# Optimization experiments

Hardware: AMD Instinct MI355X
Metric: run time of the kernel (lower is better)

Reference implementation:

```python
import jax, jax.numpy as jnp
import numpy as np

VOCAB, D_MODEL, N_STATE, H_HEADS, LAYERS = 64, 512, 32, 16, 4
EXPAND = 2
D_INNER = EXPAND * D_MODEL          # 1024
P_HEAD = D_INNER // H_HEADS         # 64
CONV_DIM = D_INNER + 2 * N_STATE    # x, B, C share the depthwise conv
K_CONV = 4
D_IN_PROJ = 2 * D_INNER + 2 * N_STATE + H_HEADS  # z, x, B, C, dt
BATCH, SEQ = 4, 1024
EPS = 1e-5


def rmsnorm(x, w):
    return x * jax.lax.rsqrt(jnp.mean(x * x, axis=-1, keepdims=True) + EPS) * w


def silu(x):
    return x * jax.nn.sigmoid(x)


def causal_depthwise_conv(x, w, b):
    # x: [B,L,C], w: [C,K], b: [C]; causal (left) padding, depthwise groups
    xt = jnp.transpose(x, (0, 2, 1))  # [B,C,L]
    out = jax.lax.conv_general_dilated(xt, w[:, None, :], (1,), [(K_CONV - 1, 0)], feature_group_count=w.shape[0])
    return jnp.transpose(out, (0, 2, 1)) + b


def ssd(xh, dt, A, Bm, Cm, Dp):
    # Mamba2 SSD recurrence. xh [B,L,H,P], dt [B,L,H], A [H], Bm/Cm [B,L,N], Dp [H]
    dA = jnp.exp(dt * A)              # decay per (batch, step, head)
    dtx = dt[..., None] * xh          # [B,L,H,P]

    def step(h, inp):
        dA_t, dtx_t, B_t, C_t = inp
        # h: [B,H,P,N]
        h = dA_t[:, :, None, None] * h + dtx_t[..., None] * B_t[:, None, None, :]
        y = jnp.einsum('bhpn,bn->bhp', h, C_t)
        return h, y

    h0 = jnp.zeros((xh.shape[0], H_HEADS, P_HEAD, N_STATE), xh.dtype)
    _, ys = jax.lax.scan(step, h0, (jnp.moveaxis(dA, 1, 0), jnp.moveaxis(dtx, 1, 0), jnp.moveaxis(Bm, 1, 0), jnp.moveaxis(Cm, 1, 0)))
    return jnp.moveaxis(ys, 0, 1) + xh * Dp[None, None, :, None]


def mamba_block(x, norm_w, W_in, b_in, conv_w, conv_b, dt_bias, A_log, Dp, gnorm_w, W_out, b_out):
    res = x
    u = rmsnorm(x, norm_w)
    zxbcdt = u @ W_in + b_in                                # [B,L,D_IN_PROJ]
    z = zxbcdt[..., :D_INNER]
    xBC = zxbcdt[..., D_INNER:D_INNER + CONV_DIM]
    dt = zxbcdt[..., D_INNER + CONV_DIM:]                   # [B,L,H]
    xBC = silu(causal_depthwise_conv(xBC, conv_w, conv_b))
    xc = xBC[..., :D_INNER]
    Bm = xBC[..., D_INNER:D_INNER + N_STATE]
    Cm = xBC[..., D_INNER + N_STATE:]
    dt = jax.nn.softplus(dt + dt_bias)
    xh = xc.reshape(xc.shape[0], xc.shape[1], H_HEADS, P_HEAD)
    y = ssd(xh, dt, -jnp.exp(A_log), Bm, Cm, Dp)
    y = y.reshape(y.shape[0], y.shape[1], D_INNER)
    y = rmsnorm(y * silu(z), gnorm_w)                       # gated RMSNorm
    return res + y @ W_out + b_out


def forward(input_tokens, emb, norm_w, W_in, b_in, conv_w, conv_b, dt_bias, A_log, D_param, gnorm_w, W_out, b_out, head_w, head_b):
    h = emb[input_tokens]
    for i in range(LAYERS):
        h = mamba_block(h, norm_w[i], W_in[i], b_in[i], conv_w[i], conv_b[i], dt_bias[i], A_log[i], D_param[i], gnorm_w[i], W_out[i], b_out[i])
    return h @ head_w + head_b


def setup_inputs() -> dict:
    key = jax.random.key(0)
    ks = jax.random.split(key, 8)
    s = 0.02
    return {
        'input_tokens': jax.random.randint(ks[0], (BATCH, SEQ), 0, VOCAB),
        'emb': jax.random.normal(ks[1], (VOCAB, D_MODEL), jnp.float32) * s,
        'norm_w': jnp.ones((LAYERS, D_MODEL), jnp.float32),
        'W_in': jax.random.normal(ks[2], (LAYERS, D_MODEL, D_IN_PROJ), jnp.float32) * s,
        'b_in': jnp.zeros((LAYERS, D_IN_PROJ), jnp.float32),
        'conv_w': jax.random.normal(ks[3], (LAYERS, CONV_DIM, K_CONV), jnp.float32) * 0.1,
        'conv_b': jnp.zeros((LAYERS, CONV_DIM), jnp.float32),
        'dt_bias': jnp.tile(jnp.log(jnp.expm1(jnp.linspace(0.001, 0.1, H_HEADS, dtype=jnp.float32))), (LAYERS, 1)),
        'A_log': jnp.tile(jnp.log(jnp.arange(1, H_HEADS + 1, dtype=jnp.float32)), (LAYERS, 1)),
        'D_param': jnp.ones((LAYERS, H_HEADS), jnp.float32),
        'gnorm_w': jnp.ones((LAYERS, D_INNER), jnp.float32),
        'W_out': jax.random.normal(ks[4], (LAYERS, D_INNER, D_MODEL), jnp.float32) * s,
        'b_out': jnp.zeros((LAYERS, D_MODEL), jnp.float32),
        'head_w': jax.random.normal(ks[5], (D_MODEL, VOCAB), jnp.float32) * s,
        'head_b': jnp.zeros((VOCAB,), jnp.float32),
    }


def reference(input_tokens, emb, norm_w, W_in, b_in, conv_w, conv_b, dt_bias, A_log, D_param, gnorm_w, W_out, b_out, head_w, head_b):
    return forward(input_tokens, emb, norm_w, W_in, b_in, conv_w, conv_b, dt_bias, A_log, D_param, gnorm_w, W_out, b_out, head_w, head_b)
```

## Files before the change

kernel.cpp:

```cpp
#include <hip/hip_runtime.h>
#include <hip/hip_bf16.h>

#define VOCAB     64
#define D_MODEL   512
#define N_STATE   32
#define H_HEADS   16
#define LAYERS    4
#define D_INNER   1024
#define P_HEAD    64
#define CONV_DIM  1088
#define K_CONV    4
#define D_IN_PROJ 2128
#define NPAD_IN   2176
#define NPAD_HEAD 64
#define BATCH     4
#define SEQ       1024
#define NTOK      (BATCH*SEQ)
#define EPS       1e-5f
#define CL        64
#define NC        (SEQ/CL)
#define PSTR      80

typedef __bf16 bf16x8 __attribute__((ext_vector_type(8)));
typedef float  f32x4  __attribute__((ext_vector_type(4)));

__device__ __forceinline__ float sigmoidf_(float x) { return 1.f / (1.f + __expf(-x)); }
__device__ __forceinline__ float softplusf_(float x) { return (x > 20.f) ? x : log1pf(__expf(x)); }

__device__ __forceinline__ void gload_lds16(const void* g, void* l) {
  __builtin_amdgcn_global_load_lds((const __attribute__((address_space(1))) void*)g,
                                   (__attribute__((address_space(3))) void*)l,
                                   16, 0, 0);
}

__global__ __launch_bounds__(256) void rmsnorm512_kernel(
    const float* __restrict__ x, const float* __restrict__ w,
    __bf16* __restrict__ out,
    const int* __restrict__ tok, const float* __restrict__ emb,
    float* __restrict__ hout) {
  int wv = threadIdx.x >> 6, lane = threadIdx.x & 63;
  int tokid = blockIdx.x * 4 + wv;
  const float* src = tok ? emb + (size_t)tok[tokid] * D_MODEL
                         : x + (size_t)tokid * D_MODEL;
  f32x4 v0 = *(const f32x4*)(src + lane * 8);
  f32x4 v1 = *(const f32x4*)(src + lane * 8 + 4);
  if (tok) {
    float* hr = hout + (size_t)tokid * D_MODEL;
    *(f32x4*)(hr + lane * 8) = v0;
    *(f32x4*)(hr + lane * 8 + 4) = v1;
  }
  float ss = v0[0]*v0[0] + v0[1]*v0[1] + v0[2]*v0[2] + v0[3]*v0[3]
           + v1[0]*v1[0] + v1[1]*v1[1] + v1[2]*v1[2] + v1[3]*v1[3];
  #pragma unroll
  for (int o = 32; o >= 1; o >>= 1) ss += __shfl_xor(ss, o);
  float sc = rsqrtf(ss * (1.f / D_MODEL) + EPS);
  f32x4 w0 = *(const f32x4*)(w + lane * 8);
  f32x4 w1 = *(const f32x4*)(w + lane * 8 + 4);
  bf16x8 o8;
  #pragma unroll
  for (int k = 0; k < 4; k++) o8[k]     = (__bf16)(v0[k] * sc * w0[k]);
  #pragma unroll
  for (int k = 0; k < 4; k++) o8[4 + k] = (__bf16)(v1[k] * sc * w1[k]);
  *(bf16x8*)(out + (size_t)tokid * D_MODEL + lane * 8) = o8;
}

__global__ __launch_bounds__(256) void transpose_all_kernel(
    const float* __restrict__ W_in, const float* __restrict__ W_out,
    const float* __restrict__ head_w,
    __bf16* __restrict__ WtIn, __bf16* __restrict__ WtOut, __bf16* __restrict__ WtHead) {
  int b = blockIdx.x;
  const float* W; __bf16* Wt; int K, N, Npad, bx, by;
  if (b < 4352) {
    int z = b / 1088, r = b % 1088;
    bx = r % 68; by = r / 68;
    W = W_in + (size_t)z * D_MODEL * D_IN_PROJ;
    Wt = WtIn + (size_t)z * NPAD_IN * D_MODEL;
    K = D_MODEL; N = D_IN_PROJ; Npad = NPAD_IN;
  } else if (b < 6400) {
    int r = b - 4352; int z = r / 512; r %= 512;
    bx = r % 16; by = r / 16;
    W = W_out + (size_t)z * D_INNER * D_MODEL;
    Wt = WtOut + (size_t)z * D_MODEL * D_INNER;
    K = D_INNER; N = D_MODEL; Npad = D_MODEL;
  } else {
    int r = b - 6400;
    bx = r % 2; by = r / 2;
    W = head_w; Wt = WtHead;
    K = D_MODEL; N = VOCAB; Npad = NPAD_HEAD;
  }
  __shared__ float T[32][33];
  int n0 = bx * 32, k0 = by * 32;
  int tx = threadIdx.x & 31, ty = threadIdx.x >> 5;
  #pragma unroll
  for (int i = 0; i < 4; i++) {
    int n = n0 + tx;
    T[ty + i * 8][tx] = (n < N) ? W[(size_t)(k0 + ty + i * 8) * N + n] : 0.f;
  }
  __syncthreads();
  #pragma unroll
  for (int i = 0; i < 4; i++)
    Wt[(size_t)(n0 + ty + i * 8) * K + k0 + tx] = (__bf16)T[tx][ty + i * 8];
}

#define TK 64
__global__ __launch_bounds__(256) void gemm_bf16_kernel(
    const __bf16* __restrict__ A, const __bf16* __restrict__ Bt,
    const float* __restrict__ bias, const float* __restrict__ res,
    float* __restrict__ C, __bf16* __restrict__ Cbf, int K, int N, int ldc) {
  __shared__ __bf16 As[64 * TK];
  __shared__ __bf16 Bs[64 * TK];
  int tid = threadIdx.x;
  int lane = tid & 63, wave = tid >> 6;
  int wm = wave >> 1, wn = wave & 1;
  int q = lane >> 4, l16 = lane & 15;
  size_t row0 = (size_t)blockIdx.y * 64;
  int col0 = blockIdx.x * 64;
  const __bf16* Ab = A + row0 * K;
  const __bf16* Bb = Bt + (size_t)col0 * K;

  f32x4 acc[2][2];
  #pragma unroll
  for (int i = 0; i < 2; i++)
    #pragma unroll
    for (int j = 0; j < 2; j++) acc[i][j] = (f32x4){0.f, 0.f, 0.f, 0.f};

  for (int k0 = 0; k0 < K; k0 += TK) {
    #pragma unroll
    for (int r = 0; r < 2; r++) {
      int lin = r * 256 + tid;
      size_t goff = (size_t)(lin >> 3) * K + k0 + (lin & 7) * 8;
      gload_lds16(Ab + goff, As + lin * 8);
      gload_lds16(Bb + goff, Bs + lin * 8);
    }
    __syncthreads();
    #pragma unroll
    for (int ks = 0; ks < 2; ks++) {
      bf16x8 af[2], bfv[2];
      #pragma unroll
      for (int i = 0; i < 2; i++)
        af[i] = *(const bf16x8*)(As + (wm * 32 + i * 16 + l16) * TK + ks * 32 + q * 8);
      #pragma unroll
      for (int j = 0; j < 2; j++)
        bfv[j] = *(const bf16x8*)(Bs + (wn * 32 + j * 16 + l16) * TK + ks * 32 + q * 8);
      #pragma unroll
      for (int i = 0; i < 2; i++)
        #pragma unroll
        for (int j = 0; j < 2; j++)
          acc[i][j] = __builtin_amdgcn_mfma_f32_16x16x32_bf16(af[i], bfv[j], acc[i][j], 0, 0, 0);
    }
    __syncthreads();
  }

  #pragma unroll
  for (int i = 0; i < 2; i++) {
    size_t mrow = row0 + wm * 32 + i * 16 + q * 4;
    #pragma unroll
    for (int j = 0; j < 2; j++) {
      int col = col0 + wn * 32 + j * 16 + l16;
      if (col < N) {
        float bv = bias ? bias[col] : 0.f;
        #pragma unroll
        for (int rr = 0; rr < 4; rr++) {
          size_t off = (mrow + rr) * (size_t)ldc + col;
          float v = acc[i][j][rr] + bv;
          if (res) v += res[off];
          if (C)   C[off] = v;
          if (Cbf) Cbf[off] = (__bf16)v;
        }
      }
    }
  }
}

__global__ __launch_bounds__(256) void gemm_bf16_128(
    const __bf16* __restrict__ A, const __bf16* __restrict__ Bt,
    const float* __restrict__ bias, __bf16* __restrict__ Cbf,
    int K, int N, int ldc) {
  __shared__ __bf16 As[128 * TK];
  __shared__ __bf16 Bs[128 * TK];
  int tid = threadIdx.x;
  int lane = tid & 63, wave = tid >> 6;
  int wm = wave >> 1, wn = wave & 1;
  int q = lane >> 4, l16 = lane & 15;
  size_t row0 = (size_t)blockIdx.y * 128;
  int col0 = blockIdx.x * 128;
  const __bf16* Ab = A + row0 * K;
  const __bf16* Bb = Bt + (size_t)col0 * K;

  f32x4 acc[4][4];
  #pragma unroll
  for (int i = 0; i < 4; i++)
    #pragma unroll
    for (int j = 0; j < 4; j++) acc[i][j] = (f32x4){0.f, 0.f, 0.f, 0.f};

  for (int k0 = 0; k0 < K; k0 += TK) {
    #pragma unroll
    for (int r = 0; r < 4; r++) {
      int lin = r * 256 + tid;
      size_t goff = (size_t)(lin >> 3) * K + k0 + (lin & 7) * 8;
      gload_lds16(Ab + goff, As + lin * 8);
      gload_lds16(Bb + goff, Bs + lin * 8);
    }
    __syncthreads();
    #pragma unroll
    for (int ks = 0; ks < 2; ks++) {
      bf16x8 af[4], bfv[4];
      #pragma unroll
      for (int i = 0; i < 4; i++)
        af[i] = *(const bf16x8*)(As + (wm * 64 + i * 16 + l16) * TK + ks * 32 + q * 8);
      #pragma unroll
      for (int j = 0; j < 4; j++)
        bfv[j] = *(const bf16x8*)(Bs + (wn * 64 + j * 16 + l16) * TK + ks * 32 + q * 8);
      #pragma unroll
      for (int i = 0; i < 4; i++)
        #pragma unroll
        for (int j = 0; j < 4; j++)
          acc[i][j] = __builtin_amdgcn_mfma_f32_16x16x32_bf16(af[i], bfv[j], acc[i][j], 0, 0, 0);
    }
    __syncthreads();
  }

  #pragma unroll
  for (int i = 0; i < 4; i++) {
    size_t mrow = row0 + wm * 64 + i * 16 + q * 4;
    #pragma unroll
    for (int j = 0; j < 4; j++) {
      int col = col0 + wn * 64 + j * 16 + l16;
      if (col < N) {
        float bv = bias[col];
        #pragma unroll
        for (int rr = 0; rr < 4; rr++)
          Cbf[(mrow + rr) * (size_t)ldc + col] = (__bf16)(acc[i][j][rr] + bv);
      }
    }
  }
}

__device__ __forceinline__ void wave0_dt_cumsum(
    const __bf16* __restrict__ zxbf, const float* __restrict__ dt_bias,
    int b, int h, int t0, int tid, float* ldt, float* lcs) {
  if (tid < 64) {
    float dv = (float)zxbf[((size_t)(b * SEQ + t0 + tid)) * D_IN_PROJ + 2 * D_INNER + 2 * N_STATE + h]
               + dt_bias[h];
    float dtv = softplusf_(dv);
    float cs = dtv;
    #pragma unroll
    for (int off = 1; off < 64; off <<= 1) {
      float o = __shfl_up(cs, off);
      if (tid >= off) cs += o;
    }
    ldt[tid] = dtv;
    lcs[tid] = cs;
  }
}

__global__ __launch_bounds__(256) void ssd_local_kernel(
    const __bf16* __restrict__ zxbf, const float* __restrict__ conv_w,
    const float* __restrict__ conv_b, const float* __restrict__ dt_bias,
    const float* __restrict__ A_log,
    float* __restrict__ Slocal, float* __restrict__ dAprod) {
  int blk = blockIdx.x;
  int c = blk % NC;
  int h = (blk / NC) % H_HEADS;
  int b = blk / (NC * H_HEADS);
  int tid = threadIdx.x;
  int lane = tid & 63, wave = tid >> 6;
  int q = lane >> 4, l16 = lane & 15;
  int t0 = c * CL;
  float A = -__expf(A_log[h]);
  __shared__ __bf16 rawbuf[68 * 64 + 68 * 32];
  __shared__ __bf16 lxT[64][PSTR];
  __shared__ __bf16 lBT[32][PSTR];
  __shared__ float ldt[64], lcs[64];
  __bf16* rawx = rawbuf;
  __bf16* rawB = rawbuf + 68 * 64;
  for (int i = tid; i < 68 * 8; i += 256) {
    int r = i >> 3, c0 = (i & 7) * 8;
    int gr = t0 - 3 + r;
    bf16x8 v;
    #pragma unroll
    for (int k = 0; k < 8; k++) v[k] = (__bf16)0.f;
    if (gr >= 0)
      v = *(const bf16x8*)(zxbf + ((size_t)(b * SEQ + gr)) * D_IN_PROJ + D_INNER + h * 64 + c0);
    *(bf16x8*)(rawx + r * 64 + c0) = v;
  }
  for (int i = tid; i < 68 * 4; i += 256) {
    int r = i >> 2, c0 = (i & 3) * 8;
    int gr = t0 - 3 + r;
    bf16x8 v;
    #pragma unroll
    for (int k = 0; k < 8; k++) v[k] = (__bf16)0.f;
    if (gr >= 0)
      v = *(const bf16x8*)(zxbf + ((size_t)(b * SEQ + gr)) * D_IN_PROJ + 2 * D_INNER + c0);
    *(bf16x8*)(rawB + r * 32 + c0) = v;
  }
  wave0_dt_cumsum(zxbf, dt_bias, b, h, t0, tid, ldt, lcs);
  __syncthreads();
  float cs63 = lcs[63];
  {
    int p = tid & 63;
    const float* w = conv_w + (h * 64 + p) * K_CONV;
    float w0 = w[0], w1 = w[1], w2 = w[2], w3 = w[3];
    float cb = conv_b[h * 64 + p];
    for (int i = tid; i < CL * 64; i += 256) {
      int t = i >> 6;
      float a = cb + w0 * (float)rawx[t * 64 + p] + w1 * (float)rawx[(t + 1) * 64 + p]
                   + w2 * (float)rawx[(t + 2) * 64 + p] + w3 * (float)rawx[(t + 3) * 64 + p];
      lxT[p][t] = (__bf16)(a * sigmoidf_(a));
    }
  }
  {
    int n = tid & 31;
    const float* w = conv_w + (D_INNER + n) * K_CONV;
    float w0 = w[0], w1 = w[1], w2 = w[2], w3 = w[3];
    float cb = conv_b[D_INNER + n];
    for (int i = tid; i < CL * 32; i += 256) {
      int t = i >> 5;
      float a = cb + w0 * (float)rawB[t * 32 + n] + w1 * (float)rawB[(t + 1) * 32 + n]
                   + w2 * (float)rawB[(t + 2) * 32 + n] + w3 * (float)rawB[(t + 3) * 32 + n];
      float v = a * sigmoidf_(a);
      float wt = ldt[t] * __expf(A * (cs63 - lcs[t]));
      lBT[n][t] = (__bf16)(v * wt);
    }
  }
  __syncthreads();
  f32x4 acc[2];
  acc[0] = (f32x4){0.f,0.f,0.f,0.f}; acc[1] = (f32x4){0.f,0.f,0.f,0.f};
  #pragma unroll
  for (int kb = 0; kb < 2; kb++) {
    bf16x8 af = *(const bf16x8*)(&lxT[wave * 16 + l16][kb * 32 + q * 8]);
    #pragma unroll
    for (int j = 0; j < 2; j++) {
      bf16x8 bf = *(const bf16x8*)(&lBT[l16 + 16 * j][kb * 32 + q * 8]);
      acc[j] = __builtin_amdgcn_mfma_f32_16x16x32_bf16(af, bf, acc[j], 0, 0, 0);
    }
  }
  float* sT = (float*)rawbuf;
  #pragma unroll
  for (int j = 0; j < 2; j++) {
    int n = l16 + 16 * j;
    #pragma unroll
    for (int rr = 0; rr < 4; rr++) {
      int p = wave * 16 + q * 4 + rr;
      sT[p * 36 + n] = acc[j][rr];
    }
  }
  {
    int row = tid >> 2, c0 = (tid & 3) * 8;
    f32x4 a = *(const f32x4*)(sT + row * 36 + c0);
    f32x4 b2 = *(const f32x4*)(sT + row * 36 + c0 + 4);
    float* dstp = Slocal + (size_t)blk * 2048 + row * 32 + c0;
    *(f32x4*)dstp = a;
    *(f32x4*)(dstp + 4) = b2;
  }
  if (tid == 0) dAprod[blk] = __expf(A * cs63);
}

__global__ __launch_bounds__(256) void ssd_out_kernel(
    const __bf16* __restrict__ zxbf, const float* __restrict__ conv_w,
    const float* __restrict__ conv_b, const float* __restrict__ dt_bias,
    const float* __restrict__ A_log, const float* __restrict__ Dp,
    const float* __restrict__ Slocal, const float* __restrict__ dAprod,
    __bf16* __restrict__ y) {
  int blk = blockIdx.x;
  int c = blk % NC;
  int h = (blk / NC) % H_HEADS;
  int b = blk / (NC * H_HEADS);
  int tid = threadIdx.x;
  int lane = tid & 63, wave = tid >> 6;
  int q = lane >> 4, l16 = lane & 15;
  int t0 = c * CL;
  float A = -__expf(A_log[h]);
  float D = Dp[h];
  __shared__ __bf16 rawbuf[2 * 68 * 64];
  __shared__ __bf16 lxT[64][PSTR];
  __shared__ __bf16 lB[64][32];
  __shared__ __bf16 lC[64][32];
  __shared__ __bf16 lS[64][32];
  __shared__ float ldt[64], lcs[64];
  __shared__ float pr[NC];
  __bf16* rawx = rawbuf;
  __bf16* rawBC = rawbuf + 68 * 64;
  for (int i = tid; i < 68 * 8; i += 256) {
    int r = i >> 3, c0 = (i & 7) * 8;
    int gr = t0 - 3 + r;
    bf16x8 vx, vbc;
    #pragma unroll
    for (int k = 0; k < 8; k++) { vx[k] = (__bf16)0.f; vbc[k] = (__bf16)0.f; }
    if (gr >= 0) {
      const __bf16* rowp = zxbf + ((size_t)(b * SEQ + gr)) * D_IN_PROJ;
      vx  = *(const bf16x8*)(rowp + D_INNER + h * 64 + c0);
      vbc = *(const bf16x8*)(rowp + 2 * D_INNER + c0);
    }
    *(bf16x8*)(rawx + r * 64 + c0)  = vx;
    *(bf16x8*)(rawBC + r * 64 + c0) = vbc;
  }
  if (tid < NC) pr[tid] = dAprod[(blk - c) + tid];
  wave0_dt_cumsum(zxbf, dt_bias, b, h, t0, tid, ldt, lcs);
  __syncthreads();
  {
    int p = tid & 63;
    const float* w = conv_w + (h * 64 + p) * K_CONV;
    float w0 = w[0], w1 = w[1], w2 = w[2], w3 = w[3];
    float cb = conv_b[h * 64 + p];
    for (int i = tid; i < CL * 64; i += 256) {
      int t = i >> 6;
      float a = cb + w0 * (float)rawx[t * 64 + p] + w1 * (float)rawx[(t + 1) * 64 + p]
                   + w2 * (float)rawx[(t + 2) * 64 + p] + w3 * (float)rawx[(t + 3) * 64 + p];
      lxT[p][t] = (__bf16)(a * sigmoidf_(a));
    }
  }
  {
    int col = tid & 63;
    const float* w = conv_w + (D_INNER + col) * K_CONV;
    float w0 = w[0], w1 = w[1], w2 = w[2], w3 = w[3];
    float cb = conv_b[D_INNER + col];
    for (int i = tid; i < CL * 64; i += 256) {
      int t = i >> 6;
      float a = cb + w0 * (float)rawBC[t * 64 + col] + w1 * (float)rawBC[(t + 1) * 64 + col]
                   + w2 * (float)rawBC[(t + 2) * 64 + col] + w3 * (float)rawBC[(t + 3) * 64 + col];
      float v = a * sigmoidf_(a);
      if (col < 32) lB[t][col] = (__bf16)v; else lC[t][col - 32] = (__bf16)v;
    }
  }
  {
    int p = tid >> 2, n0 = (tid & 3) * 8;
    const float* sl = Slocal + (size_t)(blk - c) * 2048 + p * 32 + n0;
    float st[8] = {};
    for (int j = 0; j < c; j++) {
      f32x4 a = *(const f32x4*)(sl + (size_t)j * 2048);
      f32x4 bq = *(const f32x4*)(sl + (size_t)j * 2048 + 4);
      float prj = pr[j];
      #pragma unroll
      for (int k = 0; k < 4; k++) { st[k] = prj * st[k] + a[k]; st[4 + k] = prj * st[4 + k] + bq[k]; }
    }
    #pragma unroll
    for (int k = 0; k < 8; k++) lS[p][n0 + k] = (__bf16)st[k];
  }
  __syncthreads();
  bf16x8 afC = *(const bf16x8*)(&lC[wave * 16 + l16][q * 8]);
  f32x4 accG[4], accI[4], accY[4];
  #pragma unroll
  for (int j = 0; j < 4; j++) {
    accG[j] = (f32x4){0.f,0.f,0.f,0.f};
    accI[j] = (f32x4){0.f,0.f,0.f,0.f};
    accY[j] = (f32x4){0.f,0.f,0.f,0.f};
  }
  #pragma unroll
  for (int j = 0; j < 4; j++) {
    bf16x8 bf = *(const bf16x8*)(&lB[l16 + 16 * j][q * 8]);
    accG[j] = __builtin_amdgcn_mfma_f32_16x16x32_bf16(afC, bf, accG[j], 0, 0, 0);
  }
  #pragma unroll
  for (int j = 0; j < 4; j++) {
    bf16x8 bf = *(const bf16x8*)(&lS[l16 + 16 * j][q * 8]);
    accI[j] = __builtin_amdgcn_mfma_f32_16x16x32_bf16(afC, bf, accI[j], 0, 0, 0);
  }
  __bf16* pP = rawbuf + wave * 16 * PSTR;
  #pragma unroll
  for (int j = 0; j < 4; j++) {
    int s = l16 + 16 * j;
    float css = lcs[s], dts = ldt[s];
    #pragma unroll
    for (int rr = 0; rr < 4; rr++) {
      int tl = q * 4 + rr;
      int t = wave * 16 + tl;
      float val = accG[j][rr] * __expf(A * (lcs[t] - css)) * dts;
      if (s == t) val += D;
      if (s > t) val = 0.f;
      pP[tl * PSTR + s] = (__bf16)val;
    }
  }
  #pragma unroll
  for (int kb = 0; kb < 2; kb++) {
    bf16x8 afP = *(const bf16x8*)(pP + l16 * PSTR + kb * 32 + q * 8);
    #pragma unroll
    for (int j = 0; j < 4; j++) {
      bf16x8 bf = *(const bf16x8*)(&lxT[l16 + 16 * j][kb * 32 + q * 8]);
      accY[j] = __builtin_amdgcn_mfma_f32_16x16x32_bf16(afP, bf, accY[j], 0, 0, 0);
    }
  }
  __syncthreads();
  __bf16* yT = rawbuf;
  #pragma unroll
  for (int rr = 0; rr < 4; rr++) {
    int t = wave * 16 + q * 4 + rr;
    float cumt = __expf(A * lcs[t]);
    #pragma unroll
    for (int j = 0; j < 4; j++) {
      int p = l16 + 16 * j;
      yT[t * 72 + p] = (__bf16)(accY[j][rr] + cumt * accI[j][rr]);
    }
  }
  {
    int row = tid >> 2, col0 = (tid & 3) * 16;
    bf16x8 o0 = *(const bf16x8*)(yT + row * 72 + col0);
    bf16x8 o1 = *(const bf16x8*)(yT + row * 72 + col0 + 8);
    __bf16* yrow = y + ((size_t)(b * SEQ + t0 + row)) * D_INNER + h * 64 + col0;
    *(bf16x8*)yrow = o0;
    *(bf16x8*)(yrow + 8) = o1;
  }
}

__global__ __launch_bounds__(256) void gate_norm_kernel(
    const __bf16* __restrict__ zxbf, const float* __restrict__ gw,
    const __bf16* __restrict__ y, __bf16* __restrict__ ybf) {
  int wv = threadIdx.x >> 6, lane = threadIdx.x & 63;
  int tokid = blockIdx.x * 4 + wv;
  const __bf16* zr = zxbf + (size_t)tokid * D_IN_PROJ + lane * 16;
  const __bf16* yr = y + (size_t)tokid * D_INNER + lane * 16;
  bf16x8 z0 = *(const bf16x8*)zr;
  bf16x8 z1 = *(const bf16x8*)(zr + 8);
  bf16x8 y0 = *(const bf16x8*)yr;
  bf16x8 y1 = *(const bf16x8*)(yr + 8);
  float g[16];
  float ss = 0.f;
  #pragma unroll
  for (int k = 0; k < 8; k++) {
    float zz = (float)z0[k];
    float gg = (float)y0[k] * zz * sigmoidf_(zz);
    g[k] = gg; ss += gg * gg;
  }
  #pragma unroll
  for (int k = 0; k < 8; k++) {
    float zz = (float)z1[k];
    float gg = (float)y1[k] * zz * sigmoidf_(zz);
    g[8 + k] = gg; ss += gg * gg;
  }
  #pragma unroll
  for (int o = 32; o >= 1; o >>= 1) ss += __shfl_xor(ss, o);
  float sc = rsqrtf(ss * (1.f / D_INNER) + EPS);
  f32x4 w0 = *(const f32x4*)(gw + lane * 16);
  f32x4 w1 = *(const f32x4*)(gw + lane * 16 + 4);
  f32x4 w2 = *(const f32x4*)(gw + lane * 16 + 8);
  f32x4 w3 = *(const f32x4*)(gw + lane * 16 + 12);
  bf16x8 o0, o1;
  #pragma unroll
  for (int k = 0; k < 4; k++) o0[k]     = (__bf16)(g[k]      * sc * w0[k]);
  #pragma unroll
  for (int k = 0; k < 4; k++) o0[4 + k] = (__bf16)(g[4 + k]  * sc * w1[k]);
  #pragma unroll
  for (int k = 0; k < 4; k++) o1[k]     = (__bf16)(g[8 + k]  * sc * w2[k]);
  #pragma unroll
  for (int k = 0; k < 4; k++) o1[4 + k] = (__bf16)(g[12 + k] * sc * w3[k]);
  __bf16* orow = ybf + (size_t)tokid * D_INNER + lane * 16;
  *(bf16x8*)orow = o0;
  *(bf16x8*)(orow + 8) = o1;
}

extern "C" void kernel_launch(void* const* d_in, const int* in_sizes, int n_in,
                              void* d_out, int out_size, void* d_ws, size_t ws_size,
                              hipStream_t stream) {
  const int*   tok     = (const int*)  d_in[0];
  const float* emb     = (const float*)d_in[1];
  const float* norm_w  = (const float*)d_in[2];
  const float* W_in    = (const float*)d_in[3];
  const float* b_in    = (const float*)d_in[4];
  const float* conv_w  = (const float*)d_in[5];
  const float* conv_b  = (const float*)d_in[6];
  const float* dt_bias = (const float*)d_in[7];
  const float* A_log   = (const float*)d_in[8];
  const float* D_par   = (const float*)d_in[9];
  const float* gnorm_w = (const float*)d_in[10];
  const float* W_out   = (const float*)d_in[11];
  const float* b_out   = (const float*)d_in[12];
  const float* head_w  = (const float*)d_in[13];
  const float* head_b  = (const float*)d_in[14];
  float* out = (float*)d_out;

  char* p = (char*)d_ws;
  auto alloc = [&](size_t bytes) { void* r = (void*)p; p += (bytes + 255) & ~(size_t)255; return r; };
  float*  h      = (float*) alloc((size_t)NTOK * D_MODEL * 4);
  float*  slocal = (float*) alloc((size_t)BATCH * H_HEADS * NC * P_HEAD * N_STATE * 4);
  float*  daprod = (float*) alloc((size_t)BATCH * H_HEADS * NC * 4);
  __bf16* y      = (__bf16*)alloc((size_t)NTOK * D_INNER * 2);
  __bf16* zxbf   = (__bf16*)alloc((size_t)NTOK * D_IN_PROJ * 2);
  __bf16* ubf    = (__bf16*)alloc((size_t)NTOK * D_MODEL * 2);
  __bf16* ybf    = (__bf16*)alloc((size_t)NTOK * D_INNER * 2);
  __bf16* hbf    = (__bf16*)alloc((size_t)NTOK * D_MODEL * 2);
  __bf16* WtIn   = (__bf16*)alloc((size_t)LAYERS * NPAD_IN * D_MODEL * 2);
  __bf16* WtOut  = (__bf16*)alloc((size_t)LAYERS * D_MODEL * D_INNER * 2);
  __bf16* WtHead = (__bf16*)alloc((size_t)NPAD_HEAD * D_MODEL * 2);

  transpose_all_kernel<<<6432, 256, 0, stream>>>(W_in, W_out, head_w, WtIn, WtOut, WtHead);

  for (int l = 0; l < LAYERS; l++) {
    rmsnorm512_kernel<<<NTOK / 4, 256, 0, stream>>>(
        h, norm_w + (size_t)l * D_MODEL, ubf,
        (l == 0) ? tok : nullptr, (l == 0) ? emb : nullptr, h);

    gemm_bf16_128<<<dim3(NPAD_IN / 128, NTOK / 128), 256, 0, stream>>>(
        ubf, WtIn + (size_t)l * NPAD_IN * D_MODEL, b_in + (size_t)l * D_IN_PROJ,
        zxbf, D_MODEL, D_IN_PROJ, D_IN_PROJ);

    ssd_local_kernel<<<BATCH * H_HEADS * NC, 256, 0, stream>>>(
        zxbf, conv_w + (size_t)l * CONV_DIM * K_CONV, conv_b + (size_t)l * CONV_DIM,
        dt_bias + (size_t)l * H_HEADS, A_log + (size_t)l * H_HEADS, slocal, daprod);
    ssd_out_kernel<<<BATCH * H_HEADS * NC, 256, 0, stream>>>(
        zxbf, conv_w + (size_t)l * CONV_DIM * K_CONV, conv_b + (size_t)l * CONV_DIM,
        dt_bias + (size_t)l * H_HEADS, A_log + (size_t)l * H_HEADS,
        D_par + (size_t)l * H_HEADS, slocal, daprod, y);

    gate_norm_kernel<<<NTOK / 4, 256, 0, stream>>>(zxbf, gnorm_w + (size_t)l * D_INNER, y, ybf);

    gemm_bf16_kernel<<<dim3(D_MODEL / 64, NTOK / 64), 256, 0, stream>>>(
        ybf, WtOut + (size_t)l * D_MODEL * D_INNER, b_out + (size_t)l * D_MODEL, h, h,
        (l == LAYERS - 1) ? hbf : nullptr, D_INNER, D_MODEL, D_MODEL);
  }

  gemm_bf16_kernel<<<dim3(NPAD_HEAD / 64, NTOK / 64), 256, 0, stream>>>(
      hbf, WtHead, head_b, nullptr, out, nullptr, D_MODEL, VOCAB, VOCAB);
}
```

Measured before the change: 489.4 us.

## Fold RMSNorm weights into GEMM weights and apply row scales in epilogues

```diff
diff --git a/kernel.cpp b/kernel.cpp
--- a/kernel.cpp
+++ b/kernel.cpp
@@ -33,59 +33,53 @@
                                    16, 0, 0);
 }
 
-__global__ __launch_bounds__(256) void rmsnorm512_kernel(
-    const float* __restrict__ x, const float* __restrict__ w,
-    __bf16* __restrict__ out,
+__global__ __launch_bounds__(256) void embed_kernel(
     const int* __restrict__ tok, const float* __restrict__ emb,
-    float* __restrict__ hout) {
+    float* __restrict__ h, __bf16* __restrict__ hbf, float* __restrict__ hssq) {
   int wv = threadIdx.x >> 6, lane = threadIdx.x & 63;
   int tokid = blockIdx.x * 4 + wv;
-  const float* src = tok ? emb + (size_t)tok[tokid] * D_MODEL
-                         : x + (size_t)tokid * D_MODEL;
-  f32x4 v0 = *(const f32x4*)(src + lane * 8);
-  f32x4 v1 = *(const f32x4*)(src + lane * 8 + 4);
-  if (tok) {
-    float* hr = hout + (size_t)tokid * D_MODEL;
-    *(f32x4*)(hr + lane * 8) = v0;
-    *(f32x4*)(hr + lane * 8 + 4) = v1;
-  }
+  const float* er = emb + (size_t)tok[tokid] * D_MODEL;
+  f32x4 v0 = *(const f32x4*)(er + lane * 8);
+  f32x4 v1 = *(const f32x4*)(er + lane * 8 + 4);
+  float* hr = h + (size_t)tokid * D_MODEL;
+  *(f32x4*)(hr + lane * 8) = v0;
+  *(f32x4*)(hr + lane * 8 + 4) = v1;
+  bf16x8 o8;
+  #pragma unroll
+  for (int k = 0; k < 4; k++) { o8[k] = (__bf16)v0[k]; o8[4 + k] = (__bf16)v1[k]; }
+  *(bf16x8*)(hbf + (size_t)tokid * D_MODEL + lane * 8) = o8;
   float ss = v0[0]*v0[0] + v0[1]*v0[1] + v0[2]*v0[2] + v0[3]*v0[3]
            + v1[0]*v1[0] + v1[1]*v1[1] + v1[2]*v1[2] + v1[3]*v1[3];
   #pragma unroll
   for (int o = 32; o >= 1; o >>= 1) ss += __shfl_xor(ss, o);
-  float sc = rsqrtf(ss * (1.f / D_MODEL) + EPS);
-  f32x4 w0 = *(const f32x4*)(w + lane * 8);
-  f32x4 w1 = *(const f32x4*)(w + lane * 8 + 4);
-  bf16x8 o8;
-  #pragma unroll
-  for (int k = 0; k < 4; k++) o8[k]     = (__bf16)(v0[k] * sc * w0[k]);
-  #pragma unroll
-  for (int k = 0; k < 4; k++) o8[4 + k] = (__bf16)(v1[k] * sc * w1[k]);
-  *(bf16x8*)(out + (size_t)tokid * D_MODEL + lane * 8) = o8;
+  if (lane == 0) hssq[tokid] = ss;
 }
 
 __global__ __launch_bounds__(256) void transpose_all_kernel(
     const float* __restrict__ W_in, const float* __restrict__ W_out,
     const float* __restrict__ head_w,
+    const float* __restrict__ norm_w, const float* __restrict__ gnorm_w,
     __bf16* __restrict__ WtIn, __bf16* __restrict__ WtOut, __bf16* __restrict__ WtHead) {
   int b = blockIdx.x;
-  const float* W; __bf16* Wt; int K, N, Npad, bx, by;
+  const float* W; const float* fold; __bf16* Wt; int K, N, Npad, bx, by;
   if (b < 4352) {
     int z = b / 1088, r = b % 1088;
     bx = r % 68; by = r / 68;
     W = W_in + (size_t)z * D_MODEL * D_IN_PROJ;
+    fold = norm_w + (size_t)z * D_MODEL;
     Wt = WtIn + (size_t)z * NPAD_IN * D_MODEL;
     K = D_MODEL; N = D_IN_PROJ; Npad = NPAD_IN;
   } else if (b < 6400) {
     int r = b - 4352; int z = r / 512; r %= 512;
     bx = r % 16; by = r / 16;
     W = W_out + (size_t)z * D_INNER * D_MODEL;
+    fold = gnorm_w + (size_t)z * D_INNER;
     Wt = WtOut + (size_t)z * D_MODEL * D_INNER;
     K = D_INNER; N = D_MODEL; Npad = D_MODEL;
   } else {
     int r = b - 6400;
     bx = r % 2; by = r / 2;
-    W = head_w; Wt = WtHead;
+    W = head_w; fold = nullptr; Wt = WtHead;
     K = D_MODEL; N = VOCAB; Npad = NPAD_HEAD;
   }
   __shared__ float T[32][33];
@@ -97,16 +91,19 @@
     T[ty + i * 8][tx] = (n < N) ? W[(size_t)(k0 + ty + i * 8) * N + n] : 0.f;
   }
   __syncthreads();
+  float fs = fold ? fold[k0 + tx] : 1.f;
   #pragma unroll
   for (int i = 0; i < 4; i++)
-    Wt[(size_t)(n0 + ty + i * 8) * K + k0 + tx] = (__bf16)T[tx][ty + i * 8];
+    Wt[(size_t)(n0 + ty + i * 8) * K + k0 + tx] = (__bf16)(T[tx][ty + i * 8] * fs);
 }
 
 #define TK 64
 __global__ __launch_bounds__(256) void gemm_bf16_kernel(
     const __bf16* __restrict__ A, const __bf16* __restrict__ Bt,
     const float* __restrict__ bias, const float* __restrict__ res,
-    float* __restrict__ C, __bf16* __restrict__ Cbf, int K, int N, int ldc) {
+    float* __restrict__ C, __bf16* __restrict__ Cbf,
+    const float* __restrict__ ssq, float* __restrict__ hssq_out,
+    int K, int N, int ldc) {
   __shared__ __bf16 As[64 * TK];
   __shared__ __bf16 Bs[64 * TK];
   int tid = threadIdx.x;
@@ -155,18 +152,25 @@
   for (int i = 0; i < 2; i++) {
     size_t mrow = row0 + wm * 32 + i * 16 + q * 4;
     #pragma unroll
-    for (int j = 0; j < 2; j++) {
-      int col = col0 + wn * 32 + j * 16 + l16;
-      if (col < N) {
-        float bv = bias ? bias[col] : 0.f;
-        #pragma unroll
-        for (int rr = 0; rr < 4; rr++) {
+    for (int rr = 0; rr < 4; rr++) {
+      float sc = ssq ? rsqrtf(ssq[mrow + rr] * (1.f / D_INNER) + EPS) : 1.f;
+      float rowsq = 0.f;
+      #pragma unroll
+      for (int j = 0; j < 2; j++) {
+        int col = col0 + wn * 32 + j * 16 + l16;
+        if (col < N) {
           size_t off = (mrow + rr) * (size_t)ldc + col;
-          float v = acc[i][j][rr] + bv;
+          float v = acc[i][j][rr] * sc + (bias ? bias[col] : 0.f);
           if (res) v += res[off];
           if (C)   C[off] = v;
           if (Cbf) Cbf[off] = (__bf16)v;
+          rowsq += v * v;
         }
+      }
+      if (hssq_out) {
+        #pragma unroll
+        for (int o = 1; o <= 8; o <<= 1) rowsq += __shfl_xor(rowsq, o);
+        if (l16 == 0) atomicAdd(hssq_out + mrow + rr, rowsq);
       }
     }
   }
@@ -175,7 +179,7 @@
 __global__ __launch_bounds__(256) void gemm_bf16_128(
     const __bf16* __restrict__ A, const __bf16* __restrict__ Bt,
     const float* __restrict__ bias, __bf16* __restrict__ Cbf,
-    int K, int N, int ldc) {
+    const float* __restrict__ rssq, int K, int N, int ldc) {
   __shared__ __bf16 As[128 * TK];
   __shared__ __bf16 Bs[128 * TK];
   int tid = threadIdx.x;
@@ -224,13 +228,13 @@
   for (int i = 0; i < 4; i++) {
     size_t mrow = row0 + wm * 64 + i * 16 + q * 4;
     #pragma unroll
-    for (int j = 0; j < 4; j++) {
-      int col = col0 + wn * 64 + j * 16 + l16;
-      if (col < N) {
-        float bv = bias[col];
-        #pragma unroll
-        for (int rr = 0; rr < 4; rr++)
-          Cbf[(mrow + rr) * (size_t)ldc + col] = (__bf16)(acc[i][j][rr] + bv);
+    for (int rr = 0; rr < 4; rr++) {
+      float sc = rsqrtf(rssq[mrow + rr] * (1.f / D_MODEL) + EPS);
+      #pragma unroll
+      for (int j = 0; j < 4; j++) {
+        int col = col0 + wn * 64 + j * 16 + l16;
+        if (col < N)
+          Cbf[(mrow + rr) * (size_t)ldc + col] = (__bf16)(acc[i][j][rr] * sc + bias[col]);
       }
     }
   }
@@ -258,7 +262,8 @@
     const __bf16* __restrict__ zxbf, const float* __restrict__ conv_w,
     const float* __restrict__ conv_b, const float* __restrict__ dt_bias,
     const float* __restrict__ A_log,
-    float* __restrict__ Slocal, float* __restrict__ dAprod) {
+    float* __restrict__ Slocal, float* __restrict__ dAprod,
+    float* __restrict__ hssq, float* __restrict__ ssq) {
   int blk = blockIdx.x;
   int c = blk % NC;
   int h = (blk / NC) % H_HEADS;
@@ -267,6 +272,10 @@
   int lane = tid & 63, wave = tid >> 6;
   int q = lane >> 4, l16 = lane & 15;
   int t0 = c * CL;
+  if (c == 0 && h < 2) {
+    float* tgt = (h == 0) ? hssq : ssq;
+    for (int i = tid; i < SEQ; i += 256) tgt[b * SEQ + i] = 0.f;
+  }
   float A = -__expf(A_log[h]);
   __shared__ __bf16 rawbuf[68 * 64 + 68 * 32];
   __shared__ __bf16 lxT[64][PSTR];
@@ -361,7 +370,7 @@
     const float* __restrict__ conv_b, const float* __restrict__ dt_bias,
     const float* __restrict__ A_log, const float* __restrict__ Dp,
     const float* __restrict__ Slocal, const float* __restrict__ dAprod,
-    __bf16* __restrict__ y) {
+    __bf16* __restrict__ gout, float* __restrict__ ssq) {
   int blk = blockIdx.x;
   int c = blk % NC;
   int h = (blk / NC) % H_HEADS;
@@ -494,58 +503,32 @@
   }
   {
     int row = tid >> 2, col0 = (tid & 3) * 16;
-    bf16x8 o0 = *(const bf16x8*)(yT + row * 72 + col0);
-    bf16x8 o1 = *(const bf16x8*)(yT + row * 72 + col0 + 8);
-    __bf16* yrow = y + ((size_t)(b * SEQ + t0 + row)) * D_INNER + h * 64 + col0;
-    *(bf16x8*)yrow = o0;
-    *(bf16x8*)(yrow + 8) = o1;
-  }
-}
-
-__global__ __launch_bounds__(256) void gate_norm_kernel(
-    const __bf16* __restrict__ zxbf, const float* __restrict__ gw,
-    const __bf16* __restrict__ y, __bf16* __restrict__ ybf) {
-  int wv = threadIdx.x >> 6, lane = threadIdx.x & 63;
-  int tokid = blockIdx.x * 4 + wv;
-  const __bf16* zr = zxbf + (size_t)tokid * D_IN_PROJ + lane * 16;
-  const __bf16* yr = y + (size_t)tokid * D_INNER + lane * 16;
-  bf16x8 z0 = *(const bf16x8*)zr;
-  bf16x8 z1 = *(const bf16x8*)(zr + 8);
-  bf16x8 y0 = *(const bf16x8*)yr;
-  bf16x8 y1 = *(const bf16x8*)(yr + 8);
-  float g[16];
-  float ss = 0.f;
-  #pragma unroll
-  for (int k = 0; k < 8; k++) {
-    float zz = (float)z0[k];
-    float gg = (float)y0[k] * zz * sigmoidf_(zz);
-    g[k] = gg; ss += gg * gg;
-  }
-  #pragma unroll
-  for (int k = 0; k < 8; k++) {
-    float zz = (float)z1[k];
-    float gg = (float)y1[k] * zz * sigmoidf_(zz);
-    g[8 + k] = gg; ss += gg * gg;
-  }
-  #pragma unroll
-  for (int o = 32; o >= 1; o >>= 1) ss += __shfl_xor(ss, o);
-  float sc = rsqrtf(ss * (1.f / D_INNER) + EPS);
-  f32x4 w0 = *(const f32x4*)(gw + lane * 16);
-  f32x4 w1 = *(const f32x4*)(gw + lane * 16 + 4);
-  f32x4 w2 = *(const f32x4*)(gw + lane * 16 + 8);
-  f32x4 w3 = *(const f32x4*)(gw + lane * 16 + 12);
-  bf16x8 o0, o1;
-  #pragma unroll
-  for (int k = 0; k < 4; k++) o0[k]     = (__bf16)(g[k]      * sc * w0[k]);
-  #pragma unroll
-  for (int k = 0; k < 4; k++) o0[4 + k] = (__bf16)(g[4 + k]  * sc * w1[k]);
-  #pragma unroll
-  for (int k = 0; k < 4; k++) o1[k]     = (__bf16)(g[8 + k]  * sc * w2[k]);
-  #pragma unroll
-  for (int k = 0; k < 4; k++) o1[4 + k] = (__bf16)(g[12 + k] * sc * w3[k]);
-  __bf16* orow = ybf + (size_t)tokid * D_INNER + lane * 16;
-  *(bf16x8*)orow = o0;
-  *(bf16x8*)(orow + 8) = o1;
+    bf16x8 y0 = *(const bf16x8*)(yT + row * 72 + col0);
+    bf16x8 y1 = *(const bf16x8*)(yT + row * 72 + col0 + 8);
+    const __bf16* zrow = zxbf + ((size_t)(b * SEQ + t0 + row)) * D_IN_PROJ + h * 64 + col0;
+    bf16x8 z0 = *(const bf16x8*)zrow;
+    bf16x8 z1 = *(const bf16x8*)(zrow + 8);
+    bf16x8 g0, g1;
+    float ss = 0.f;
+    #pragma unroll
+    for (int k = 0; k < 8; k++) {
+      float zz = (float)z0[k];
+      float gg = (float)y0[k] * zz * sigmoidf_(zz);
+      g0[k] = (__bf16)gg; ss += gg * gg;
+    }
+    #pragma unroll
+    for (int k = 0; k < 8; k++) {
+      float zz = (float)z1[k];
+      float gg = (float)y1[k] * zz * sigmoidf_(zz);
+      g1[k] = (__bf16)gg; ss += gg * gg;
+    }
+    __bf16* grow = gout + ((size_t)(b * SEQ + t0 + row)) * D_INNER + h * 64 + col0;
+    *(bf16x8*)grow = g0;
+    *(bf16x8*)(grow + 8) = g1;
+    ss += __shfl_xor(ss, 1);
+    ss += __shfl_xor(ss, 2);
+    if ((tid & 3) == 0) atomicAdd(ssq + b * SEQ + t0 + row, ss);
+  }
 }
 
 extern "C" void kernel_launch(void* const* d_in, const int* in_sizes, int n_in,
@@ -573,41 +556,39 @@
   float*  h      = (float*) alloc((size_t)NTOK * D_MODEL * 4);
   float*  slocal = (float*) alloc((size_t)BATCH * H_HEADS * NC * P_HEAD * N_STATE * 4);
   float*  daprod = (float*) alloc((size_t)BATCH * H_HEADS * NC * 4);
-  __bf16* y      = (__bf16*)alloc((size_t)NTOK * D_INNER * 2);
+  float*  hssq   = (float*) alloc((size_t)NTOK * 4);
+  float*  ssq    = (float*) alloc((size_t)NTOK * 4);
   __bf16* zxbf   = (__bf16*)alloc((size_t)NTOK * D_IN_PROJ * 2);
-  __bf16* ubf    = (__bf16*)alloc((size_t)NTOK * D_MODEL * 2);
-  __bf16* ybf    = (__bf16*)alloc((size_t)NTOK * D_INNER * 2);
+  __bf16* gbf    = (__bf16*)alloc((size_t)NTOK * D_INNER * 2);
   __bf16* hbf    = (__bf16*)alloc((size_t)NTOK * D_MODEL * 2);
   __bf16* WtIn   = (__bf16*)alloc((size_t)LAYERS * NPAD_IN * D_MODEL * 2);
   __bf16* WtOut  = (__bf16*)alloc((size_t)LAYERS * D_MODEL * D_INNER * 2);
   __bf16* WtHead = (__bf16*)alloc((size_t)NPAD_HEAD * D_MODEL * 2);
 
-  transpose_all_kernel<<<6432, 256, 0, stream>>>(W_in, W_out, head_w, WtIn, WtOut, WtHead);
+  transpose_all_kernel<<<6432, 256, 0, stream>>>(
+      W_in, W_out, head_w, norm_w, gnorm_w, WtIn, WtOut, WtHead);
+
+  embed_kernel<<<NTOK / 4, 256, 0, stream>>>(tok, emb, h, hbf, hssq);
 
   for (int l = 0; l < LAYERS; l++) {
-    rmsnorm512_kernel<<<NTOK / 4, 256, 0, stream>>>(
-        h, norm_w + (size_t)l * D_MODEL, ubf,
-        (l == 0) ? tok : nullptr, (l == 0) ? emb : nullptr, h);
-
     gemm_bf16_128<<<dim3(NPAD_IN / 128, NTOK / 128), 256, 0, stream>>>(
-        ubf, WtIn + (size_t)l * NPAD_IN * D_MODEL, b_in + (size_t)l * D_IN_PROJ,
-        zxbf, D_MODEL, D_IN_PROJ, D_IN_PROJ);
+        hbf, WtIn + (size_t)l * NPAD_IN * D_MODEL, b_in + (size_t)l * D_IN_PROJ,
+        zxbf, hssq, D_MODEL, D_IN_PROJ, D_IN_PROJ);
 
     ssd_local_kernel<<<BATCH * H_HEADS * NC, 256, 0, stream>>>(
         zxbf, conv_w + (size_t)l * CONV_DIM * K_CONV, conv_b + (size_t)l * CONV_DIM,
-        dt_bias + (size_t)l * H_HEADS, A_log + (size_t)l * H_HEADS, slocal, daprod);
+        dt_bias + (size_t)l * H_HEADS, A_log + (size_t)l * H_HEADS, slocal, daprod,
+        hssq, ssq);
     ssd_out_kernel<<<BATCH * H_HEADS * NC, 256, 0, stream>>>(
         zxbf, conv_w + (size_t)l * CONV_DIM * K_CONV, conv_b + (size_t)l * CONV_DIM,
         dt_bias + (size_t)l * H_HEADS, A_log + (size_t)l * H_HEADS,
-        D_par + (size_t)l * H_HEADS, slocal, daprod, y);
-
-    gate_norm_kernel<<<NTOK / 4, 256, 0, stream>>>(zxbf, gnorm_w + (size_t)l * D_INNER, y, ybf);
+        D_par + (size_t)l * H_HEADS, slocal, daprod, gbf, ssq);
 
     gemm_bf16_kernel<<<dim3(D_MODEL / 64, NTOK / 64), 256, 0, stream>>>(
-        ybf, WtOut + (size_t)l * D_MODEL * D_INNER, b_out + (size_t)l * D_MODEL, h, h,
-        (l == LAYERS - 1) ? hbf : nullptr, D_INNER, D_MODEL, D_MODEL);
+        gbf, WtOut + (size_t)l * D_MODEL * D_INNER, b_out + (size_t)l * D_MODEL, h,
+        h, hbf, ssq, hssq, D_INNER, D_MODEL, D_MODEL);
   }
 
   gemm_bf16_kernel<<<dim3(NPAD_HEAD / 64, NTOK / 64), 256, 0, stream>>>(
-      hbf, WtHead, head_b, nullptr, out, nullptr, D_MODEL, VOCAB, VOCAB);
-}
+      hbf, WtHead, head_b, nullptr, out, nullptr, nullptr, nullptr, D_MODEL, VOCAB, VOCAB);
+}
```

After: 557.6 us. 1.14x slower.
